# Optimization experiments

Hardware: AMD Instinct MI355X
Metric: run time of the kernel (lower is better)

The kernel has to match this reference:

```python
import jax, jax.numpy as jnp
import numpy as np

TOL = 0.0
MARGIN = 0.0
REVERSE = False
SIZE_AVERAGE = True

N, C, H, W = 128, 256, 32, 64


def setup_inputs() -> dict:
    key = jax.random.key(0)
    k1, k2 = jax.random.split(key)
    raw_feat = jax.random.normal(k1, (N, C, H, W), dtype=jnp.float32)
    rectified_feat = jax.random.normal(k2, (N, C, H, W), dtype=jnp.float32)
    return {"raw_feat": raw_feat, "rectified_feat": rectified_feat}


def _rank(feat):
    # feat: [n, c, h, w] -> channel mean -> [n, h, w]
    n, c, h, w = feat.shape
    m = jnp.mean(feat, axis=1)                       # [n, h, w]
    flat = m.reshape(n, -1)
    nrm = jnp.linalg.norm(flat, axis=1, keepdims=True)
    normed = (flat / nrm).reshape(n, h, w)
    # batched singular values of small h x w matrices
    s = jnp.linalg.svd(normed, compute_uv=False)     # [n, min(h,w)]
    return jnp.sum((s > TOL).astype(jnp.float32), axis=1)  # [n]


def reference(raw_feat, rectified_feat):
    rank1 = _rank(raw_feat)
    rank2 = _rank(rectified_feat)
    y = jnp.full_like(rank1, -1.0 if REVERSE else 1.0)
    # margin ranking loss: max(0, -y*(x1-x2)+margin), no per-element reduction
    loss = jnp.maximum(0.0, -y * (rank1 - rank2) + MARGIN)
    if SIZE_AVERAGE:
        loss = jnp.sum(loss) / raw_feat.shape[0]
    return loss
```

## Files before the change

### kernel.cpp

```cpp
#include <hip/hip_runtime.h>
#include <math.h>


#define N_BATCH 128
#define C_CH    256
#define H_DIM   32
#define W_DIM   64
#define HW      (H_DIM * W_DIM)
#define HW4     (HW / 4)

template <int CHUNKS>
__global__ __launch_bounds__(512) void channel_sum_kernel(
    const float* __restrict__ raw, const float* __restrict__ rect,
    float* __restrict__ part )
{
    const int CPR = C_CH / CHUNKS;
    int b     = blockIdx.x;
    int chunk = b % CHUNKS;
    int plane = b / CHUNKS;
    int input = plane >> 7;
    int n     = plane & 127;

    const float* src = input ? rect : raw;
    const float4* p = (const float4*)(src +
        ((size_t)n * C_CH + (size_t)chunk * CPR) * HW) + threadIdx.x;

    float4 acc = make_float4(0.f, 0.f, 0.f, 0.f);
#pragma unroll 1
    for (int cb = 0; cb < CPR; cb += 8) {
        float4 x0 = p[(cb + 0) * HW4];
        float4 x1 = p[(cb + 1) * HW4];
        float4 x2 = p[(cb + 2) * HW4];
        float4 x3 = p[(cb + 3) * HW4];
        float4 x4 = p[(cb + 4) * HW4];
        float4 x5 = p[(cb + 5) * HW4];
        float4 x6 = p[(cb + 6) * HW4];
        float4 x7 = p[(cb + 7) * HW4];
        acc.x += ((x0.x + x1.x) + (x2.x + x3.x)) + ((x4.x + x5.x) + (x6.x + x7.x));
        acc.y += ((x0.y + x1.y) + (x2.y + x3.y)) + ((x4.y + x5.y) + (x6.y + x7.y));
        acc.z += ((x0.z + x1.z) + (x2.z + x3.z)) + ((x4.z + x5.z) + (x6.z + x7.z));
        acc.w += ((x0.w + x1.w) + (x2.w + x3.w)) + ((x4.w + x5.w) + (x6.w + x7.w));
    }
    ((float4*)part)[(size_t)b * 512 + threadIdx.x] = acc;
}

template <int CHUNKS>
__global__ __launch_bounds__(64) void rank_kernel(
    const float* __restrict__ part, float* __restrict__ ranks)
{
    int mat = blockIdx.x;
    int t   = threadIdx.x;
    const float* base = part + (size_t)mat * CHUNKS * HW;

    float a[H_DIM];
#pragma unroll
    for (int i = 0; i < H_DIM; ++i) {
        float s = 0.0f;
#pragma unroll
        for (int k = 0; k < CHUNKS; ++k)
            s += base[k * HW + i * W_DIM + t];
        a[i] = s;
    }

    unsigned used = 0;
    int rank = 0;
    for (int c = 0; c < W_DIM; ++c) {
        float v[H_DIM];
#pragma unroll
        for (int i = 0; i < H_DIM; ++i) v[i] = __shfl(a[i], c);

        float best = 0.0f; int p = -1;
#pragma unroll
        for (int i = 0; i < H_DIM; ++i) {
            float av = fabsf(v[i]);
            bool cand = (((used >> i) & 1u) == 0u) && (av > best);
            best = cand ? av : best;
            p    = cand ? i  : p;
        }
        if (p >= 0) {
            used |= (1u << p);
            ++rank;
            float ap = 0.0f, vp = 1.0f;
#pragma unroll
            for (int i = 0; i < H_DIM; ++i) {
                if (i == p) { ap = a[i]; vp = v[i]; }
            }
            float inv = 1.0f / vp;
#pragma unroll
            for (int i = 0; i < H_DIM; ++i) {
                if (((used >> i) & 1u) == 0u) a[i] -= (v[i] * inv) * ap;
            }
            if (rank == H_DIM) break;
        }
    }
    if (t == 0) ranks[mat] = (float)rank;
}

__global__ __launch_bounds__(128) void loss_kernel(
    const float* __restrict__ ranks, float* __restrict__ out)
{
    __shared__ float red[128];
    int t = threadIdx.x;
    float r1 = ranks[t];
    float r2 = ranks[N_BATCH + t];
    red[t] = fmaxf(0.0f, -(r1 - r2));
    __syncthreads();
    for (int s = 64; s > 0; s >>= 1) {
        if (t < s) red[t] += red[t + s];
        __syncthreads();
    }
    if (t == 0) out[0] = red[0] / (float)N_BATCH;
}

extern "C" void kernel_launch(void* const* d_in, const int* in_sizes, int n_in,
                              void* d_out, int out_size, void* d_ws, size_t ws_size,
                              hipStream_t stream)
{
    const float* raw  = (const float*)d_in[0];
    const float* rect = (const float*)d_in[1];
    float* out = (float*)d_out;
    float* part = (float*)d_ws;

    const size_t need4 = (size_t)2 * N_BATCH * 4 * HW * sizeof(float) + 1024;
    if (ws_size >= need4) {
        float* ranks = part + (size_t)2 * N_BATCH * 4 * HW;
        channel_sum_kernel<4><<<2 * N_BATCH * 4, 512, 0, stream>>>(raw, rect, part);
        rank_kernel<4><<<2 * N_BATCH, 64, 0, stream>>>(part, ranks);
        loss_kernel<<<1, 128, 0, stream>>>(ranks, out);
    } else {
        float* ranks = part + (size_t)2 * N_BATCH * HW;
        channel_sum_kernel<1><<<2 * N_BATCH, 512, 0, stream>>>(raw, rect, part);
        rank_kernel<1><<<2 * N_BATCH, 64, 0, stream>>>(part, ranks);
        loss_kernel<<<1, 128, 0, stream>>>(ranks, out);
    }
}
```

Baseline: 144.3 us.

## Assign per-wave channel chunks in channel sum and pick partial count by workspace size

The channel-sum kernel now gives each 64-lane wave a full spatial plane over a contiguous channel chunk. Each lane keeps eight independent float4 accumulators instead of tree-adding eight channels per iteration. The launcher picks 16, 8, 4 or 1 partial sums per plane according to available workspace, with the aim of more independent loads in flight and finer work distribution. In exchange, more partials means extra partial-buffer writes and extra reads in the rank kernel, and fewer total waves run.

```diff
diff --git a/kernel.cpp b/kernel.cpp
--- a/kernel.cpp
+++ b/kernel.cpp
@@ -9,55 +9,63 @@
 #define HW      (H_DIM * W_DIM)
 #define HW4     (HW / 4)
 
-template <int CHUNKS>
+template <int CPW>
 __global__ __launch_bounds__(512) void channel_sum_kernel(
     const float* __restrict__ raw, const float* __restrict__ rect,
     float* __restrict__ part )
 {
-    const int CPR = C_CH / CHUNKS;
-    int b     = blockIdx.x;
-    int chunk = b % CHUNKS;
-    int plane = b / CHUNKS;
+    const int CPC = C_CH / CPW;
+    int wid  = blockIdx.x * 8 + (threadIdx.x >> 6);
+    int lane = threadIdx.x & 63;
+    int plane = wid / CPW;
+    int chunk = wid % CPW;
     int input = plane >> 7;
     int n     = plane & 127;
 
-    const float* src = input ? rect : raw;
-    const float4* p = (const float4*)(src +
-        ((size_t)n * C_CH + (size_t)chunk * CPR) * HW) + threadIdx.x;
+    const float4* q = (const float4*)(input ? rect : raw)
+                    + ((size_t)n * C_CH + (size_t)chunk * CPC) * HW4 + lane;
 
-    float4 acc = make_float4(0.f, 0.f, 0.f, 0.f);
+    float4 a0 = make_float4(0,0,0,0), a1 = a0, a2 = a0, a3 = a0;
+    float4 a4 = a0, a5 = a0, a6 = a0, a7 = a0;
 #pragma unroll 1
-    for (int cb = 0; cb < CPR; cb += 8) {
-        float4 x0 = p[(cb + 0) * HW4];
-        float4 x1 = p[(cb + 1) * HW4];
-        float4 x2 = p[(cb + 2) * HW4];
-        float4 x3 = p[(cb + 3) * HW4];
-        float4 x4 = p[(cb + 4) * HW4];
-        float4 x5 = p[(cb + 5) * HW4];
-        float4 x6 = p[(cb + 6) * HW4];
-        float4 x7 = p[(cb + 7) * HW4];
-        acc.x += ((x0.x + x1.x) + (x2.x + x3.x)) + ((x4.x + x5.x) + (x6.x + x7.x));
-        acc.y += ((x0.y + x1.y) + (x2.y + x3.y)) + ((x4.y + x5.y) + (x6.y + x7.y));
-        acc.z += ((x0.z + x1.z) + (x2.z + x3.z)) + ((x4.z + x5.z) + (x6.z + x7.z));
-        acc.w += ((x0.w + x1.w) + (x2.w + x3.w)) + ((x4.w + x5.w) + (x6.w + x7.w));
+    for (int c = 0; c < CPC; ++c) {
+        const float4* r = q + (size_t)c * HW4;
+        float4 x0 = r[0 * 64];
+        float4 x1 = r[1 * 64];
+        float4 x2 = r[2 * 64];
+        float4 x3 = r[3 * 64];
+        float4 x4 = r[4 * 64];
+        float4 x5 = r[5 * 64];
+        float4 x6 = r[6 * 64];
+        float4 x7 = r[7 * 64];
+        a0.x += x0.x; a0.y += x0.y; a0.z += x0.z; a0.w += x0.w;
+        a1.x += x1.x; a1.y += x1.y; a1.z += x1.z; a1.w += x1.w;
+        a2.x += x2.x; a2.y += x2.y; a2.z += x2.z; a2.w += x2.w;
+        a3.x += x3.x; a3.y += x3.y; a3.z += x3.z; a3.w += x3.w;
+        a4.x += x4.x; a4.y += x4.y; a4.z += x4.z; a4.w += x4.w;
+        a5.x += x5.x; a5.y += x5.y; a5.z += x5.z; a5.w += x5.w;
+        a6.x += x6.x; a6.y += x6.y; a6.z += x6.z; a6.w += x6.w;
+        a7.x += x7.x; a7.y += x7.y; a7.z += x7.z; a7.w += x7.w;
     }
-    ((float4*)part)[(size_t)b * 512 + threadIdx.x] = acc;
+    float4* o = (float4*)part + (size_t)wid * HW4 + lane;
+    o[0 * 64] = a0; o[1 * 64] = a1; o[2 * 64] = a2; o[3 * 64] = a3;
+    o[4 * 64] = a4; o[5 * 64] = a5; o[6 * 64] = a6; o[7 * 64] = a7;
 }
 
-template <int CHUNKS>
+template <int CPW>
 __global__ __launch_bounds__(64) void rank_kernel(
     const float* __restrict__ part, float* __restrict__ ranks)
 {
     int mat = blockIdx.x;
     int t   = threadIdx.x;
-    const float* base = part + (size_t)mat * CHUNKS * HW;
+    const float* base = part + (size_t)mat * CPW * HW;
 
     float a[H_DIM];
 #pragma unroll
     for (int i = 0; i < H_DIM; ++i) {
         float s = 0.0f;
 #pragma unroll
-        for (int k = 0; k < CHUNKS; ++k)
+        for (int k = 0; k < CPW; ++k)
             s += base[k * HW + i * W_DIM + t];
         a[i] = s;
     }
@@ -112,6 +120,17 @@
     if (t == 0) out[0] = red[0] / (float)N_BATCH;
 }
 
+template <int CPW>
+static void run_path(const float* raw, const float* rect, float* ws,
+                     float* out, hipStream_t stream)
+{
+    float* part  = ws;
+    float* ranks = part + (size_t)2 * N_BATCH * CPW * HW;
+    channel_sum_kernel<CPW><<<32 * CPW, 512, 0, stream>>>(raw, rect, part);
+    rank_kernel<CPW><<<2 * N_BATCH, 64, 0, stream>>>(part, ranks);
+    loss_kernel<<<1, 128, 0, stream>>>(ranks, out);
+}
+
 extern "C" void kernel_launch(void* const* d_in, const int* in_sizes, int n_in,
                               void* d_out, int out_size, void* d_ws, size_t ws_size,
                               hipStream_t stream)
@@ -119,18 +138,13 @@
     const float* raw  = (const float*)d_in[0];
     const float* rect = (const float*)d_in[1];
     float* out = (float*)d_out;
-    float* part = (float*)d_ws;
+    float* ws  = (float*)d_ws;
 
-    const size_t need4 = (size_t)2 * N_BATCH * 4 * HW * sizeof(float) + 1024;
-    if (ws_size >= need4) {
-        float* ranks = part + (size_t)2 * N_BATCH * 4 * HW;
-        channel_sum_kernel<4><<<2 * N_BATCH * 4, 512, 0, stream>>>(raw, rect, part);
-        rank_kernel<4><<<2 * N_BATCH, 64, 0, stream>>>(part, ranks);
-        loss_kernel<<<1, 128, 0, stream>>>(ranks, out);
-    } else {
-        float* ranks = part + (size_t)2 * N_BATCH * HW;
-        channel_sum_kernel<1><<<2 * N_BATCH, 512, 0, stream>>>(raw, rect, part);
-        rank_kernel<1><<<2 * N_BATCH, 64, 0, stream>>>(part, ranks);
-        loss_kernel<<<1, 128, 0, stream>>>(ranks, out);
-    }
+    auto need = [](int cpw) {
+        return (size_t)2 * N_BATCH * cpw * HW * sizeof(float) + 4096;
+    };
+    if      (ws_size >= need(16)) run_path<16>(raw, rect, ws, out, stream);
+    else if (ws_size >= need(8))  run_path<8>(raw, rect, ws, out, stream);
+    else if (ws_size >= need(4))  run_path<4>(raw, rect, ws, out, stream);
+    else                          run_path<1>(raw, rect, ws, out, stream);
 }
```

Result: slower. 164.5 us (+14.0%).
